# Kernel tuning notes

Measured on AMD Instinct MI355X. Metric: run time of the kernel, lower is better.

The kernel has to match this reference:

```python
import jax, jax.numpy as jnp
import numpy as np

B, N, F = 16, 256, 64
H = 64  # MLP hidden width


def setup_inputs() -> dict:
    key = jax.random.key(0)
    k_h, k_w1, k_w2 = jax.random.split(key, 3)
    hidden_state = jax.random.normal(k_h, (B, N, F), dtype=jnp.float32)
    # nn.init.normal_(weight, 0.0, 0.01); bias = 0
    w1 = jax.random.normal(k_w1, (H, 2 * F), dtype=jnp.float32) * 0.01  # Linear(128, 64)
    b1 = jnp.zeros((H,), dtype=jnp.float32)
    w2 = jax.random.normal(k_w2, (1, H), dtype=jnp.float32) * 0.01  # Linear(64, 1)
    b2 = jnp.zeros((1,), dtype=jnp.float32)
    return {"hidden_state": hidden_state, "w1": w1, "b1": b1, "w2": w2, "b2": b2}


def reference(hidden_state, w1, b1, w2, b2):
    # hidden_state: [B, N, F]. Pair (i, j) feature = cat(h_i, h_j) -> MLP -> sigmoid.
    # Split first linear: cat(h_i, h_j) @ W1^T == h_i @ W1a^T + h_j @ W1b^T.
    Bsz, Nn, Fd = hidden_state.shape
    w1a, w1b = w1[:, :Fd], w1[:, Fd:]                      # [H, F] each
    a = jnp.einsum('bnf,hf->bnh', hidden_state, w1a)       # [B, N, H] (i-part)
    c = jnp.einsum('bnf,hf->bnh', hidden_state, w1b)       # [B, N, H] (j-part)
    z = jax.nn.relu(a[:, :, None, :] + c[:, None, :, :] + b1)  # [B, N, N, H]
    logits = jnp.einsum('bijh,oh->bijo', z, w2)[..., 0] + b2[0]  # [B, N, N]
    adj = jax.nn.sigmoid(logits)
    # Diagonal entries are never overwritten -> stay 1.
    eye = jnp.eye(Nn, dtype=adj.dtype)
    return adj * (1.0 - eye) + eye
```

## Files before the change

kernel.cpp:

```cpp
#include <hip/hip_runtime.h>
#include <hip/hip_bf16.h>
#include <hip/hip_fp16.h>


#define Nn 256
#define Fd 64
#define Hd 64

typedef _Float16 h2v    __attribute__((ext_vector_type(2)));
typedef __fp16   fp16x2 __attribute__((ext_vector_type(2)));
typedef _Float16 f16x8  __attribute__((ext_vector_type(8)));
typedef float    f32x4  __attribute__((ext_vector_type(4)));
union H2   { h2v v; fp16x2 p; unsigned int u; };
union U4F8 { uint4 u; f16x8 v; };
union HS1  { _Float16 h; unsigned short s; };

__global__ __launch_bounds__(256) void fused_kernel(
    const float* __restrict__ hs, const float* __restrict__ w1,
    const float* __restrict__ b1, const float* __restrict__ w2,
    const float* __restrict__ b2, float* __restrict__ out) {
  __shared__ uint2 w1s[64][32];
  __shared__ uint2 hsI[64][16];
  __shared__ uint2 hsJ[64][16];
  __shared__ uint4 aT[64][8];
  __shared__ uint4 cT[64][8];
  __shared__ unsigned int w2h[32];

  const int t  = threadIdx.x;
  const int b  = blockIdx.z;
  const int i0 = blockIdx.y * 64;
  const int j0 = blockIdx.x * 64;

  {
    const float4* w14 = (const float4*)w1;
#pragma unroll
    for (int p = 0; p < 8; ++p) {
      const int k4 = p * 256 + t;
      const int r = k4 >> 5, col4 = k4 & 31;
      const float4 v = w14[k4];
      H2 lo, hi;
      lo.p = __builtin_amdgcn_cvt_pkrtz(v.x, v.y);
      hi.p = __builtin_amdgcn_cvt_pkrtz(v.z, v.w);
      const int cc = col4 >> 1, hf = col4 & 1;
      w1s[r][((cc ^ (r & 15)) << 1) | hf] = make_uint2(lo.u, hi.u);
    }
  }
  {
    const float4* hi4 = (const float4*)(hs + (size_t)(b * Nn + i0) * Fd);
    const float4* hj4 = (const float4*)(hs + (size_t)(b * Nn + j0) * Fd);
#pragma unroll
    for (int p = 0; p < 4; ++p) {
      const int k4 = p * 256 + t;
      const int r = k4 >> 4, col4 = k4 & 15;
      const int cc = col4 >> 1, hf = col4 & 1;
      const int idx = ((cc ^ (r & 7)) << 1) | hf;
      {
        const float4 v = hi4[k4];
        H2 lo, hi_;
        lo.p  = __builtin_amdgcn_cvt_pkrtz(v.x, v.y);
        hi_.p = __builtin_amdgcn_cvt_pkrtz(v.z, v.w);
        hsI[r][idx] = make_uint2(lo.u, hi_.u);
      }
      {
        const float4 v = hj4[k4];
        H2 lo, hi_;
        lo.p  = __builtin_amdgcn_cvt_pkrtz(v.x, v.y);
        hi_.p = __builtin_amdgcn_cvt_pkrtz(v.z, v.w);
        hsJ[r][idx] = make_uint2(lo.u, hi_.u);
      }
    }
  }
  if (t < 32) {
    H2 wv2;
    wv2.v = (h2v){(_Float16)w2[2 * t], (_Float16)w2[2 * t + 1]};
    w2h[t] = wv2.u;
  }
  __syncthreads();

  {
    const int l   = t & 63;
    const int w   = t >> 6;
    const int l15 = l & 15, l4 = l >> 4;
    const int mrow = w * 16 + l15;

    f32x4 acca[4] = {{0,0,0,0},{0,0,0,0},{0,0,0,0},{0,0,0,0}};
    f32x4 accc[4] = {{0,0,0,0},{0,0,0,0},{0,0,0,0},{0,0,0,0}};

#pragma unroll
    for (int s = 0; s < 2; ++s) {
      U4F8 afI, afJ;
      afI.u = ((const uint4*)&hsI[mrow][0])[(s * 4 + l4) ^ (mrow & 7)];
      afJ.u = ((const uint4*)&hsJ[mrow][0])[(s * 4 + l4) ^ (mrow & 7)];
#pragma unroll
      for (int nt = 0; nt < 4; ++nt) {
        const int rh = nt * 16 + l15;
        U4F8 bfa, bfc;
        bfa.u = ((const uint4*)&w1s[rh][0])[(s * 4 + l4) ^ (rh & 15)];
        bfc.u = ((const uint4*)&w1s[rh][0])[(8 + s * 4 + l4) ^ (rh & 15)];
        acca[nt] = __builtin_amdgcn_mfma_f32_16x16x32_f16(afI.v, bfa.v, acca[nt], 0, 0, 0);
        accc[nt] = __builtin_amdgcn_mfma_f32_16x16x32_f16(afJ.v, bfc.v, accc[nt], 0, 0, 0);
      }
    }

    __syncthreads();

    unsigned short* aTh = (unsigned short*)aT;
    unsigned short* cTh = (unsigned short*)cT;
#pragma unroll
    for (int nt = 0; nt < 4; ++nt) {
      const int n = nt * 16 + l15;
      const float bval = b1[n];
      const int chunk = n >> 3, pos = n & 7;
#pragma unroll
      for (int i = 0; i < 4; ++i) {
        const int row = w * 16 + l4 * 4 + i;
        const int sw = chunk ^ ((row >> 2) & 7);
        HS1 xa; xa.h = (_Float16)(acca[nt][i] + bval);
        aTh[row * 64 + sw * 8 + pos] = xa.s;
        HS1 xc; xc.h = (_Float16)(accc[nt][i]);
        cTh[row * 64 + sw * 8 + pos] = xc.s;
      }
    }
  }
  __syncthreads();

  const int jt = t & 15;
  const int it = t >> 4;
  const int ib = it * 4;
  const int jb = jt * 4;
  const int sa = it & 7;
  const int sc = jt & 7;

  const uint4* w2q = (const uint4*)w2h;

  float acc[4][4] = {{0.f}};

#pragma unroll 2
  for (int h8 = 0; h8 < 8; ++h8) {
    const uint4 wwu = w2q[h8];
    uint4 av[4], cv[4];
#pragma unroll
    for (int u = 0; u < 4; ++u) av[u] = aT[ib + u][h8 ^ sa];
#pragma unroll
    for (int v = 0; v < 4; ++v) cv[v] = cT[jb + v][h8 ^ sc];

#pragma unroll
    for (int u = 0; u < 4; ++u) {
      const unsigned au4[4] = {av[u].x, av[u].y, av[u].z, av[u].w};
#pragma unroll
      for (int v = 0; v < 4; ++v) {
        const unsigned cu4[4] = {cv[v].x, cv[v].y, cv[v].z, cv[v].w};
        const unsigned wu4[4] = {wwu.x, wwu.y, wwu.z, wwu.w};
#pragma unroll
        for (int m = 0; m < 4; ++m) {
          H2 za, zc, zw;
          za.u = au4[m]; zc.u = cu4[m]; zw.u = wu4[m];
          h2v z = __builtin_elementwise_max(za.v + zc.v, (h2v)(_Float16)0);
#if __has_builtin(__builtin_amdgcn_fdot2)
          acc[u][v] = __builtin_amdgcn_fdot2(z, zw.v, acc[u][v], false);
#else
          acc[u][v] = fmaf((float)z.x, (float)zw.v.x, acc[u][v]);
          acc[u][v] = fmaf((float)z.y, (float)zw.v.y, acc[u][v]);
#endif
        }
      }
    }
  }

  const float bias2 = b2[0];
#pragma unroll
  for (int u = 0; u < 4; ++u) {
    const int i = i0 + ib + u;
    float4 o;
    o.x = (i == j0 + jb + 0) ? 1.0f : 1.f / (1.f + __expf(-(acc[u][0] + bias2)));
    o.y = (i == j0 + jb + 1) ? 1.0f : 1.f / (1.f + __expf(-(acc[u][1] + bias2)));
    o.z = (i == j0 + jb + 2) ? 1.0f : 1.f / (1.f + __expf(-(acc[u][2] + bias2)));
    o.w = (i == j0 + jb + 3) ? 1.0f : 1.f / (1.f + __expf(-(acc[u][3] + bias2)));
    ((float4*)(out + (size_t)(b * Nn + i) * Nn + j0))[jt] = o;
  }
}

extern "C" void kernel_launch(void* const* d_in, const int* in_sizes, int n_in,
                              void* d_out, int out_size, void* d_ws, size_t ws_size,
                              hipStream_t stream) {
  const float* hs = (const float*)d_in[0];
  const float* w1 = (const float*)d_in[1];
  const float* b1 = (const float*)d_in[2];
  const float* w2 = (const float*)d_in[3];
  const float* b2 = (const float*)d_in[4];
  float* out = (float*)d_out;

  dim3 grid(Nn / 64, Nn / 64, 16);
  fused_kernel<<<grid, 256, 0, stream>>>(hs, w1, b1, w2, b2, out);
}
```

Measured before the change: 13.04 us.

## Double block to 512 threads, splitting projection GEMMs and pair tiles across warps

Raises the block size from 256 to 512 threads. In the projection phase, warps 0-3 compute the i-part (a) and warps 4-7 compute the j-part (c) instead of every warp doing both, which removes the intermediate __syncthreads. In the pairwise phase each thread now handles a 2x4 output tile instead of 4x4. This adds parallelism and latency hiding within each block and cuts per-thread work and registers. The cost is more threads per block, fewer output elements per thread, and some reuse of the cT loads lost across i rows.

```diff
diff --git a/kernel.cpp b/kernel.cpp
--- a/kernel.cpp
+++ b/kernel.cpp
@@ -15,7 +15,7 @@
 union U4F8 { uint4 u; f16x8 v; };
 union HS1  { _Float16 h; unsigned short s; };
 
-__global__ __launch_bounds__(256) void fused_kernel(
+__global__ __launch_bounds__(512) void fused_kernel(
     const float* __restrict__ hs, const float* __restrict__ w1,
     const float* __restrict__ b1, const float* __restrict__ w2,
     const float* __restrict__ b2, float* __restrict__ out) {
@@ -34,8 +34,8 @@
   {
     const float4* w14 = (const float4*)w1;
 #pragma unroll
-    for (int p = 0; p < 8; ++p) {
-      const int k4 = p * 256 + t;
+    for (int p = 0; p < 4; ++p) {
+      const int k4 = p * 512 + t;
       const int r = k4 >> 5, col4 = k4 & 31;
       const float4 v = w14[k4];
       H2 lo, hi;
@@ -49,8 +49,8 @@
     const float4* hi4 = (const float4*)(hs + (size_t)(b * Nn + i0) * Fd);
     const float4* hj4 = (const float4*)(hs + (size_t)(b * Nn + j0) * Fd);
 #pragma unroll
-    for (int p = 0; p < 4; ++p) {
-      const int k4 = p * 256 + t;
+    for (int p = 0; p < 2; ++p) {
+      const int k4 = p * 512 + t;
       const int r = k4 >> 4, col4 = k4 & 15;
       const int cc = col4 >> 1, hf = col4 & 1;
       const int idx = ((cc ^ (r & 7)) << 1) | hf;
@@ -80,72 +80,68 @@
   {
     const int l   = t & 63;
     const int w   = t >> 6;
+    const bool isA = (w < 4);
+    const int wv  = w & 3;
     const int l15 = l & 15, l4 = l >> 4;
-    const int mrow = w * 16 + l15;
+    const int mrow = wv * 16 + l15;
 
-    f32x4 acca[4] = {{0,0,0,0},{0,0,0,0},{0,0,0,0},{0,0,0,0}};
-    f32x4 accc[4] = {{0,0,0,0},{0,0,0,0},{0,0,0,0},{0,0,0,0}};
+    const uint2 (*hsX)[16] = isA ? hsI : hsJ;
+    const int cbase = isA ? 0 : 8;
+
+    f32x4 acc1[4] = {{0,0,0,0},{0,0,0,0},{0,0,0,0},{0,0,0,0}};
 
 #pragma unroll
     for (int s = 0; s < 2; ++s) {
-      U4F8 afI, afJ;
-      afI.u = ((const uint4*)&hsI[mrow][0])[(s * 4 + l4) ^ (mrow & 7)];
-      afJ.u = ((const uint4*)&hsJ[mrow][0])[(s * 4 + l4) ^ (mrow & 7)];
+      U4F8 af;
+      af.u = ((const uint4*)&hsX[mrow][0])[(s * 4 + l4) ^ (mrow & 7)];
 #pragma unroll
       for (int nt = 0; nt < 4; ++nt) {
         const int rh = nt * 16 + l15;
-        U4F8 bfa, bfc;
-        bfa.u = ((const uint4*)&w1s[rh][0])[(s * 4 + l4) ^ (rh & 15)];
-        bfc.u = ((const uint4*)&w1s[rh][0])[(8 + s * 4 + l4) ^ (rh & 15)];
-        acca[nt] = __builtin_amdgcn_mfma_f32_16x16x32_f16(afI.v, bfa.v, acca[nt], 0, 0, 0);
-        accc[nt] = __builtin_amdgcn_mfma_f32_16x16x32_f16(afJ.v, bfc.v, accc[nt], 0, 0, 0);
+        U4F8 bf;
+        bf.u = ((const uint4*)&w1s[rh][0])[(cbase + s * 4 + l4) ^ (rh & 15)];
+        acc1[nt] = __builtin_amdgcn_mfma_f32_16x16x32_f16(af.v, bf.v, acc1[nt], 0, 0, 0);
       }
     }
 
-    __syncthreads();
-
-    unsigned short* aTh = (unsigned short*)aT;
-    unsigned short* cTh = (unsigned short*)cT;
+    unsigned short* dTh = isA ? (unsigned short*)aT : (unsigned short*)cT;
 #pragma unroll
     for (int nt = 0; nt < 4; ++nt) {
       const int n = nt * 16 + l15;
-      const float bval = b1[n];
+      const float bval = isA ? b1[n] : 0.f;
       const int chunk = n >> 3, pos = n & 7;
 #pragma unroll
       for (int i = 0; i < 4; ++i) {
-        const int row = w * 16 + l4 * 4 + i;
+        const int row = wv * 16 + l4 * 4 + i;
         const int sw = chunk ^ ((row >> 2) & 7);
-        HS1 xa; xa.h = (_Float16)(acca[nt][i] + bval);
-        aTh[row * 64 + sw * 8 + pos] = xa.s;
-        HS1 xc; xc.h = (_Float16)(accc[nt][i]);
-        cTh[row * 64 + sw * 8 + pos] = xc.s;
+        HS1 x; x.h = (_Float16)(acc1[nt][i] + bval);
+        dTh[row * 64 + sw * 8 + pos] = x.s;
       }
     }
   }
   __syncthreads();
 
-  const int jt = t & 15;
-  const int it = t >> 4;
-  const int ib = it * 4;
-  const int jb = jt * 4;
-  const int sa = it & 7;
-  const int sc = jt & 7;
+  const int jt  = t & 15;
+  const int it2 = t >> 4;
+  const int ib  = it2 * 2;
+  const int jb  = jt * 4;
+  const int sa  = (it2 >> 1) & 7;
+  const int sc  = jt & 7;
 
   const uint4* w2q = (const uint4*)w2h;
 
-  float acc[4][4] = {{0.f}};
+  float acc[2][4] = {{0.f}};
 
 #pragma unroll 2
   for (int h8 = 0; h8 < 8; ++h8) {
     const uint4 wwu = w2q[h8];
-    uint4 av[4], cv[4];
+    uint4 av[2], cv[4];
 #pragma unroll
-    for (int u = 0; u < 4; ++u) av[u] = aT[ib + u][h8 ^ sa];
+    for (int u = 0; u < 2; ++u) av[u] = aT[ib + u][h8 ^ sa];
 #pragma unroll
     for (int v = 0; v < 4; ++v) cv[v] = cT[jb + v][h8 ^ sc];
 
 #pragma unroll
-    for (int u = 0; u < 4; ++u) {
+    for (int u = 0; u < 2; ++u) {
       const unsigned au4[4] = {av[u].x, av[u].y, av[u].z, av[u].w};
 #pragma unroll
       for (int v = 0; v < 4; ++v) {
@@ -169,7 +165,7 @@
 
   const float bias2 = b2[0];
 #pragma unroll
-  for (int u = 0; u < 4; ++u) {
+  for (int u = 0; u < 2; ++u) {
     const int i = i0 + ib + u;
     float4 o;
     o.x = (i == j0 + jb + 0) ? 1.0f : 1.f / (1.f + __expf(-(acc[u][0] + bias2)));
@@ -191,5 +187,5 @@
   float* out = (float*)d_out;
 
   dim3 grid(Nn / 64, Nn / 64, 16);
-  fused_kernel<<<grid, 256, 0, stream>>>(hs, w1, b1, w2, b2, out);
+  fused_kernel<<<grid, 512, 0, stream>>>(hs, w1, b1, w2, b2, out);
 }
```

Result: faster. 12.06 us (median of 2 runs) (-7.5%).
